# Optimization experiments

Measured on AMD Instinct MI355X. Metric: run time of the kernel, lower is better.

Reference implementation:

```python
import jax, jax.numpy as jnp
import numpy as np

N_NODES = 100000
N_EDGES = 400000
DIM = 128


def setup_inputs() -> dict:
    key = jax.random.key(0)
    ks = jax.random.split(key, 9)
    x = jax.random.normal(ks[0], (N_NODES, DIM), dtype=jnp.float32)
    edge_index3 = jax.random.randint(ks[1], (2, N_EDGES), 0, N_NODES, dtype=jnp.int64)
    edge_attr3 = jax.random.normal(ks[2], (N_EDGES, 16), dtype=jnp.float32)
    edge_attr4 = jax.random.normal(ks[3], (N_EDGES, 16), dtype=jnp.float32)
    batch = jnp.zeros((N_NODES,), dtype=jnp.int64)
    # torch Linear weights: [out_features, in_features]
    W1 = jax.random.normal(ks[4], (6 * DIM, 3 * DIM), dtype=jnp.float32) / np.sqrt(3 * DIM)
    b1 = jax.random.normal(ks[5], (6 * DIM,), dtype=jnp.float32) * 0.01
    W2 = jax.random.normal(ks[6], (1, 6 * DIM), dtype=jnp.float32) / np.sqrt(6 * DIM)
    b2 = jax.random.normal(ks[7], (1,), dtype=jnp.float32) * 0.01
    return {"x": x, "edge_index3": edge_index3, "edge_attr3": edge_attr3,
            "edge_attr4": edge_attr4, "batch": batch,
            "W1": W1, "b1": b1, "W2": W2, "b2": b2}


def reference(x, edge_index3, edge_attr3, edge_attr4, batch, W1, b1, W2, b2):
    # gather edge endpoint features: [E, DIM] each
    t0 = x[edge_index3[0]]
    t1 = x[edge_index3[1]]
    # mean over the 2 endpoints, elementwise product, squared difference -> [E, 3*DIM]
    feat = jnp.concatenate([(t0 + t1) * 0.5, t0 * t1, (t0 - t1) ** 2], axis=1)
    h = jax.nn.relu(feat @ W1.T + b1)          # [E, 6*DIM]
    yhat = (h @ W2.T + b2)[:, 0]               # [E]
    return yhat
```

## Files before the change

kernel.cpp:

```cpp
#include <hip/hip_runtime.h>

#define EDGES 400000
#define DIM 128

typedef __attribute__((ext_vector_type(8))) short bf16x8;
typedef __attribute__((ext_vector_type(4))) float f32x4;

__device__ __forceinline__ short f2bf(float f) {
    unsigned u = __builtin_bit_cast(unsigned, f);
    unsigned r = (u + 0x7fffu + ((u >> 16) & 1u)) >> 16;
    return (short)r;
}

__global__ void prep_w1(const float* __restrict__ W1, short* __restrict__ W1f) {
    int idx = blockIdx.x * 256 + threadIdx.x;
    int j    = idx & 7;
    int lane = (idx >> 3) & 63;
    int fs   = idx >> 9;
    int s    = fs % 12;
    int nt   = fs / 12;
    int n = nt * 16 + (lane & 15);
    int k = s * 32 + (lane >> 4) * 8 + j;
    W1f[idx] = f2bf(W1[n * 384 + k]);
}

#define MSTEP(S)                                                                          \
    {                                                                                     \
        bf16x8 bf = bp[((S) << 6) + lane];                                                \
        acc0 = __builtin_amdgcn_mfma_f32_16x16x32_bf16(afrag[0][(S)], bf, acc0, 0, 0, 0); \
        acc1 = __builtin_amdgcn_mfma_f32_16x16x32_bf16(afrag[1][(S)], bf, acc1, 0, 0, 0); \
    }

#define KLOOP(R)                                                            \
    MSTEP(((R) + 0) % 12)  MSTEP(((R) + 1) % 12)  MSTEP(((R) + 2) % 12)     \
    MSTEP(((R) + 3) % 12)  MSTEP(((R) + 4) % 12)  MSTEP(((R) + 5) % 12)     \
    MSTEP(((R) + 6) % 12)  MSTEP(((R) + 7) % 12)  MSTEP(((R) + 8) % 12)     \
    MSTEP(((R) + 9) % 12)  MSTEP(((R) + 10) % 12) MSTEP(((R) + 11) % 12)

__global__ __launch_bounds__(256, 2)
void edge_mlp(const float* __restrict__ x,
              const int*   __restrict__ ei,
              const float* __restrict__ b1,
              const float* __restrict__ W2,
              const float* __restrict__ b2p,
              const short* __restrict__ W1f,
              float* __restrict__ out)
{
    __shared__ short sB[2][12 * 512];

    const int tid  = threadIdx.x;
    const int lane = tid & 63;
    const int wave = tid >> 6;
    const int m    = lane & 15;
    const int quad = lane >> 4;
    const int eb   = blockIdx.x * 128;

    #pragma unroll
    for (int jj = 0; jj < 3; ++jj) {
        int s = wave * 3 + jj;
        __builtin_amdgcn_global_load_lds(
            (const __attribute__((address_space(1))) void*)(W1f + (s << 9) + lane * 8),
            (__attribute__((address_space(3))) void*)(&sB[0][s << 9]),
            16, 0, 0);
    }

    bf16x8 afrag[2][12];
    #pragma unroll
    for (int T = 0; T < 2; ++T) {
        int e = eb + wave * 32 + T * 16 + m;
        const float* r0 = x + (size_t)ei[e] * DIM;
        const float* r1 = x + (size_t)ei[EDGES + e] * DIM;
        #pragma unroll
        for (int i = 0; i < 4; ++i) {
            int c = i * 32 + quad * 8;
            f32x4 a0 = *(const f32x4*)(r0 + c);
            f32x4 a1 = *(const f32x4*)(r0 + c + 4);
            f32x4 c0 = *(const f32x4*)(r1 + c);
            f32x4 c1 = *(const f32x4*)(r1 + c + 4);
            bf16x8 fm, fp, fd;
            #pragma unroll
            for (int j = 0; j < 4; ++j) {
                float aa = a0[j], bb = c0[j];
                fm[j] = f2bf((aa + bb) * 0.5f);
                fp[j] = f2bf(aa * bb);
                float dd = aa - bb;
                fd[j] = f2bf(dd * dd);
                aa = a1[j]; bb = c1[j];
                fm[j + 4] = f2bf((aa + bb) * 0.5f);
                fp[j + 4] = f2bf(aa * bb);
                dd = aa - bb;
                fd[j + 4] = f2bf(dd * dd);
            }
            afrag[T][i]     = fm;
            afrag[T][i + 4] = fp;
            afrag[T][i + 8] = fd;
        }
    }

    float yp0[4] = {0.f, 0.f, 0.f, 0.f};
    float yp1[4] = {0.f, 0.f, 0.f, 0.f};

    __syncthreads();

    for (int nt = 0; nt < 48; ++nt) {
        const int cur = nt & 1;

        if (nt + 1 < 48) {
            const short* src = W1f + (size_t)(nt + 1) * 6144;
            #pragma unroll
            for (int jj = 0; jj < 3; ++jj) {
                int s = wave * 3 + jj;
                __builtin_amdgcn_global_load_lds(
                    (const __attribute__((address_space(1))) void*)(src + (s << 9) + lane * 8),
                    (__attribute__((address_space(3))) void*)(&sB[cur ^ 1][s << 9]),
                    16, 0, 0);
            }
        }

        f32x4 acc0 = {0.f, 0.f, 0.f, 0.f};
        f32x4 acc1 = {0.f, 0.f, 0.f, 0.f};
        const bf16x8* bp = (const bf16x8*)sB[cur];

        __builtin_amdgcn_s_setprio(1);
        switch (wave) {
            case 0: { KLOOP(0) } break;
            case 1: { KLOOP(3) } break;
            case 2: { KLOOP(6) } break;
            default: { KLOOP(9) } break;
        }
        __builtin_amdgcn_s_setprio(0);

        int ng = nt * 16 + m;
        float bias = b1[ng];
        float w2v  = W2[ng];
        #pragma unroll
        for (int r = 0; r < 4; ++r) {
            float h0 = acc0[r] + bias;
            float h1 = acc1[r] + bias;
            yp0[r] = fmaf(fmaxf(h0, 0.f), w2v, yp0[r]);
            yp1[r] = fmaf(fmaxf(h1, 0.f), w2v, yp1[r]);
        }

        __syncthreads();
    }

    #pragma unroll
    for (int off = 8; off >= 1; off >>= 1) {
        #pragma unroll
        for (int r = 0; r < 4; ++r) {
            yp0[r] += __shfl_xor(yp0[r], off, 64);
            yp1[r] += __shfl_xor(yp1[r], off, 64);
        }
    }
    if (m == 0) {
        float b2v = b2p[0];
        int e0 = eb + wave * 32 + quad * 4;
        #pragma unroll
        for (int r = 0; r < 4; ++r) {
            out[e0 + r]      = yp0[r] + b2v;
            out[e0 + 16 + r] = yp1[r] + b2v;
        }
    }
}

extern "C" void kernel_launch(void* const* d_in, const int* in_sizes, int n_in,
                              void* d_out, int out_size, void* d_ws, size_t ws_size,
                              hipStream_t stream) {
    const float* x  = (const float*)d_in[0];
    const int*   ei = (const int*)  d_in[1];
    const float* W1 = (const float*)d_in[5];
    const float* b1 = (const float*)d_in[6];
    const float* W2 = (const float*)d_in[7];
    const float* b2 = (const float*)d_in[8];
    short* W1f = (short*)d_ws;
    float* out = (float*)d_out;

    prep_w1<<<1152, 256, 0, stream>>>(W1, W1f);
    edge_mlp<<<3125, 256, 0, stream>>>(x, ei, b1, W2, b2, W1f, out);
}
```

Measured before the change: 402.2 us.

## Load W1 fragments directly from global memory instead of LDS double-buffering

Removes the shared-memory double buffer for W1 tiles along with its async global-to-LDS copies, per-iteration barriers, priority hints and wave-staggered k ordering. Each wave now reads its bf16 B fragments straight from global memory (served from L2/L1, since all blocks read the same 576 KB of W1) inside a plain unrolled k loop. The launch bounds no longer request two blocks per CU. This drops the barrier synchronisation and LDS traffic, but puts global-memory latency on every MFMA step and may change register allocation and occupancy.

Result: slower. 1.125 ms (+179.7%).

```diff
diff --git a/kernel.cpp b/kernel.cpp
--- a/kernel.cpp
+++ b/kernel.cpp
@@ -24,20 +24,7 @@
     W1f[idx] = f2bf(W1[n * 384 + k]);
 }
 
-#define MSTEP(S)                                                                          \
-    {                                                                                     \
-        bf16x8 bf = bp[((S) << 6) + lane];                                                \
-        acc0 = __builtin_amdgcn_mfma_f32_16x16x32_bf16(afrag[0][(S)], bf, acc0, 0, 0, 0); \
-        acc1 = __builtin_amdgcn_mfma_f32_16x16x32_bf16(afrag[1][(S)], bf, acc1, 0, 0, 0); \
-    }
-
-#define KLOOP(R)                                                            \
-    MSTEP(((R) + 0) % 12)  MSTEP(((R) + 1) % 12)  MSTEP(((R) + 2) % 12)     \
-    MSTEP(((R) + 3) % 12)  MSTEP(((R) + 4) % 12)  MSTEP(((R) + 5) % 12)     \
-    MSTEP(((R) + 6) % 12)  MSTEP(((R) + 7) % 12)  MSTEP(((R) + 8) % 12)     \
-    MSTEP(((R) + 9) % 12)  MSTEP(((R) + 10) % 12) MSTEP(((R) + 11) % 12)
-
-__global__ __launch_bounds__(256, 2)
+__global__ __launch_bounds__(256)
 void edge_mlp(const float* __restrict__ x,
               const int*   __restrict__ ei,
               const float* __restrict__ b1,
@@ -46,23 +33,12 @@
               const short* __restrict__ W1f,
               float* __restrict__ out)
 {
-    __shared__ short sB[2][12 * 512];
-
     const int tid  = threadIdx.x;
     const int lane = tid & 63;
     const int wave = tid >> 6;
     const int m    = lane & 15;
     const int quad = lane >> 4;
     const int eb   = blockIdx.x * 128;
-
-    #pragma unroll
-    for (int jj = 0; jj < 3; ++jj) {
-        int s = wave * 3 + jj;
-        __builtin_amdgcn_global_load_lds(
-            (const __attribute__((address_space(1))) void*)(W1f + (s << 9) + lane * 8),
-            (__attribute__((address_space(3))) void*)(&sB[0][s << 9]),
-            16, 0, 0);
-    }
 
     bf16x8 afrag[2][12];
     #pragma unroll
@@ -100,35 +76,18 @@
     float yp0[4] = {0.f, 0.f, 0.f, 0.f};
     float yp1[4] = {0.f, 0.f, 0.f, 0.f};
 
-    __syncthreads();
+    const bf16x8* __restrict__ wb = (const bf16x8*)W1f;
 
     for (int nt = 0; nt < 48; ++nt) {
-        const int cur = nt & 1;
-
-        if (nt + 1 < 48) {
-            const short* src = W1f + (size_t)(nt + 1) * 6144;
-            #pragma unroll
-            for (int jj = 0; jj < 3; ++jj) {
-                int s = wave * 3 + jj;
-                __builtin_amdgcn_global_load_lds(
-                    (const __attribute__((address_space(1))) void*)(src + (s << 9) + lane * 8),
-                    (__attribute__((address_space(3))) void*)(&sB[cur ^ 1][s << 9]),
-                    16, 0, 0);
-            }
-        }
-
         f32x4 acc0 = {0.f, 0.f, 0.f, 0.f};
         f32x4 acc1 = {0.f, 0.f, 0.f, 0.f};
-        const bf16x8* bp = (const bf16x8*)sB[cur];
-
-        __builtin_amdgcn_s_setprio(1);
-        switch (wave) {
-            case 0: { KLOOP(0) } break;
-            case 1: { KLOOP(3) } break;
-            case 2: { KLOOP(6) } break;
-            default: { KLOOP(9) } break;
+        const bf16x8* bp = wb + (nt * 12 << 6) + lane;
+        #pragma unroll
+        for (int s = 0; s < 12; ++s) {
+            bf16x8 bfrag = bp[s << 6];
+            acc0 = __builtin_amdgcn_mfma_f32_16x16x32_bf16(afrag[0][s], bfrag, acc0, 0, 0, 0);
+            acc1 = __builtin_amdgcn_mfma_f32_16x16x32_bf16(afrag[1][s], bfrag, acc1, 0, 0, 0);
         }
-        __builtin_amdgcn_s_setprio(0);
 
         int ng = nt * 16 + m;
         float bias = b1[ng];
@@ -140,8 +99,6 @@
             yp0[r] = fmaf(fmaxf(h0, 0.f), w2v, yp0[r]);
             yp1[r] = fmaf(fmaxf(h1, 0.f), w2v, yp1[r]);
         }
-
-        __syncthreads();
     }
 
     #pragma unroll
```
